# Kernel tuning notes

Hardware: AMD Instinct MI355X
Metric: run time of the kernel (lower is better)

The kernel has to match this reference:

```python
import jax, jax.numpy as jnp
import numpy as np

N_CELLS = 500_000
B = 512
D_X = 128
D_Z = 32
D_IN = D_X + D_Z  # 160
H = 256
D_OUT = 16


def _linear_params(key, fan_in, fan_out):
    k1, k2 = jax.random.split(key)
    bound = 1.0 / np.sqrt(fan_in)
    W = jax.random.uniform(k1, (fan_in, fan_out), jnp.float32, -bound, bound)
    b = jax.random.uniform(k2, (fan_out,), jnp.float32, -bound, bound)
    return W, b


def setup_inputs() -> dict:
    key = jax.random.key(0)
    ks = jax.random.split(key, 8)
    X = jax.random.uniform(ks[0], (N_CELLS, D_X), jnp.float32)  # nonneg counts-like
    Z = jax.random.normal(ks[1], (B, D_Z), jnp.float32)
    cell_to_batch = jax.random.randint(ks[2], (N_CELLS,), 0, B, jnp.int64)
    sample_idx_batch = jnp.arange(B, dtype=jnp.int64)
    W1, b1 = _linear_params(ks[3], D_IN, H)
    W2, b2 = _linear_params(ks[4], H, H)
    W3, b3 = _linear_params(ks[5], H, D_OUT)
    return {"X": X, "Z": Z, "W1": W1, "b1": b1, "W2": W2, "b2": b2,
            "W3": W3, "b3": b3, "cell_to_batch": cell_to_batch,
            "sample_idx_batch": sample_idx_batch}


def reference(X, Z, W1, b1, W2, b2, W3, b3, cell_to_batch, sample_idx_batch):
    # gather per-sample covariates to per-cell rows
    Zc = Z[cell_to_batch]                              # [N, D_Z]
    seg = sample_idx_batch[cell_to_batch]              # [N] remapped sample ids
    # preprocessor: log-normalize X, concat covariates
    Xp = jnp.concatenate([jnp.log1p(X), Zc], axis=-1)  # [N, D_IN]
    # cell predictor MLP (Linear-ReLU x2 + Linear)
    h = jax.nn.relu(Xp @ W1 + b1)
    h = jax.nn.relu(h @ W2 + b2)
    X_cell = h @ W3 + b3                               # [N, D_OUT]
    # aggregator: segment mean over cells of each sample
    nseg = sample_idx_batch.shape[0]
    sums = jax.ops.segment_sum(X_cell, seg, num_segments=nseg)
    counts = jax.ops.segment_sum(jnp.ones((X_cell.shape[0], 1), X_cell.dtype), seg, num_segments=nseg)
    Y_sample = sums / jnp.maximum(counts, 1.0)
    # postprocessor: identity
    return Y_sample
```

## Files before the change

### kernel.cpp

```cpp
#include <hip/hip_runtime.h>
#include <hip/hip_bf16.h>

typedef __attribute__((ext_vector_type(8))) short short8;
typedef __attribute__((ext_vector_type(4))) short short4v;
typedef __attribute__((ext_vector_type(4))) float floatx4;

#define N_CELLS  500000
#define B_SAMP   512
#define D_X      128
#define D_Z      32
#define D_IN     160
#define H_DIM    256
#define D_OUT    16

#define M_TILE   64
#define NBLK     7813
#define LDH      264

#define NREP     64

#define OFF_W1P   0
#define OFF_W2P   81920
#define OFF_W3P   212992
#define OFF_ACC   221184
#define OFF_CNT   2318336

#define ZERO_BLKS 2176
#define W1_BLKS   160
#define W2_BLKS   256
#define W3_BLKS   16

__device__ __forceinline__ short bfb(float x) {
    union { __hip_bfloat16 h; short s; } u;
    u.h = __float2bfloat16(x);
    return u.s;
}

__global__ __launch_bounds__(256)
void prep(const float* __restrict__ W1, const float* __restrict__ W2,
          const float* __restrict__ W3,
          __hip_bfloat16* __restrict__ w1p, __hip_bfloat16* __restrict__ w2p,
          __hip_bfloat16* __restrict__ w3p, float* __restrict__ accs) {
    int bid = blockIdx.x;
    if (bid < ZERO_BLKS) {
        accs[bid * 256 + threadIdx.x] = 0.0f;
        return;
    }
    const float* W; __hip_bfloat16* dst; int N, kS, idx, scaleK;
    if (bid < ZERO_BLKS + W1_BLKS) {
        idx = (bid - ZERO_BLKS) * 256 + threadIdx.x;
        W = W1; dst = w1p; N = H_DIM; kS = 5; scaleK = 128;
    } else if (bid < ZERO_BLKS + W1_BLKS + W2_BLKS) {
        idx = (bid - ZERO_BLKS - W1_BLKS) * 256 + threadIdx.x;
        W = W2; dst = w2p; N = H_DIM; kS = 8; scaleK = 0;
    } else {
        idx = (bid - ZERO_BLKS - W1_BLKS - W2_BLKS) * 256 + threadIdx.x;
        W = W3; dst = w3p; N = D_OUT; kS = 8; scaleK = 0;
    }
    int j = idx & 7;
    int L = (idx >> 3) & 63;
    int s = (idx >> 9) % kS;
    int t = idx / (kS << 9);
    int k = s * 32 + ((L >> 4) << 3) + j;
    int n = t * 16 + (L & 15);
    float v = W[(size_t)k * N + n];
    if (k < scaleK) v *= 0.6931471805599453f;
    dst[idx] = __float2bfloat16(v);
}

__global__ __launch_bounds__(512, 4)
void fused_mlp(const float* __restrict__ X, const float* __restrict__ Z,
               const int* __restrict__ c2b, const int* __restrict__ sidx,
               const float* __restrict__ b1, const float* __restrict__ b2,
               const float* __restrict__ b3,
               const __hip_bfloat16* __restrict__ w1p,
               const __hip_bfloat16* __restrict__ w2p,
               const __hip_bfloat16* __restrict__ w3p,
               float* __restrict__ accs, float* __restrict__ cnts) {
    __shared__ __hip_bfloat16 sA[M_TILE][LDH];
    __shared__ __hip_bfloat16 sB[M_TILE][LDH];

    const int tid = threadIdx.x;
    const int w   = tid >> 6;
    const int L   = tid & 63;
    const int q   = L >> 4;
    const int ln  = L & 15;
    const int wm  = w >> 2;
    const int wn  = w & 3;
    const int base = blockIdx.x * M_TILE;

#pragma unroll
    for (int i = 0; i < 4; ++i) {
        int idx = tid + i * 512;
        int row = idx >> 5;
        int c4  = idx & 31;
        int gr = base + row; if (gr >= N_CELLS) gr = N_CELLS - 1;
        float4 v = *(const float4*)(X + (size_t)gr * D_X + c4 * 4);
        short4v pk;
        pk.x = bfb(__log2f(1.0f + v.x));
        pk.y = bfb(__log2f(1.0f + v.y));
        pk.z = bfb(__log2f(1.0f + v.z));
        pk.w = bfb(__log2f(1.0f + v.w));
        *(short4v*)&sA[row][c4 * 4] = pk;
    }
    {
        int row = tid >> 3;
        int c0  = (tid & 7) * 4;
        int gr = base + row; if (gr >= N_CELLS) gr = N_CELLS - 1;
        int b  = c2b[gr];
        float4 v = *(const float4*)(Z + (size_t)b * D_Z + c0);
        short4v pk;
        pk.x = bfb(v.x); pk.y = bfb(v.y); pk.z = bfb(v.z); pk.w = bfb(v.w);
        *(short4v*)&sA[row][D_X + c0] = pk;
    }
    __syncthreads();

    floatx4 acc[2][4];

#pragma unroll
    for (int nt = 0; nt < 4; ++nt) {
        float4 bv = *(const float4*)(b1 + wn * 64 + nt * 16 + q * 4);
        acc[0][nt] = (floatx4){bv.x, bv.y, bv.z, bv.w};
        acc[1][nt] = acc[0][nt];
    }
#pragma unroll
    for (int s = 0; s < 5; ++s) {
        short8 x0 = *(const short8*)&sA[wm * 32 + ln][s * 32 + q * 8];
        short8 x1 = *(const short8*)&sA[wm * 32 + 16 + ln][s * 32 + q * 8];
#pragma unroll
        for (int nt = 0; nt < 4; ++nt) {
            int t = wn * 4 + nt;
            short8 wf = *(const short8*)(w1p + (size_t)(((t * 5 + s) << 6) + L) * 8);
            acc[0][nt] = __builtin_amdgcn_mfma_f32_16x16x32_bf16(wf, x0, acc[0][nt], 0, 0, 0);
            acc[1][nt] = __builtin_amdgcn_mfma_f32_16x16x32_bf16(wf, x1, acc[1][nt], 0, 0, 0);
        }
    }
#pragma unroll
    for (int mt = 0; mt < 2; ++mt)
#pragma unroll
        for (int nt = 0; nt < 4; ++nt) {
            short4v pk;
            pk.x = bfb(fmaxf(acc[mt][nt][0], 0.0f));
            pk.y = bfb(fmaxf(acc[mt][nt][1], 0.0f));
            pk.z = bfb(fmaxf(acc[mt][nt][2], 0.0f));
            pk.w = bfb(fmaxf(acc[mt][nt][3], 0.0f));
            *(short4v*)&sB[wm * 32 + mt * 16 + ln][wn * 64 + nt * 16 + q * 4] = pk;
        }
    __syncthreads();

#pragma unroll
    for (int nt = 0; nt < 4; ++nt) {
        float4 bv = *(const float4*)(b2 + wn * 64 + nt * 16 + q * 4);
        acc[0][nt] = (floatx4){bv.x, bv.y, bv.z, bv.w};
        acc[1][nt] = acc[0][nt];
    }
#pragma unroll
    for (int s = 0; s < 8; ++s) {
        short8 x0 = *(const short8*)&sB[wm * 32 + ln][s * 32 + q * 8];
        short8 x1 = *(const short8*)&sB[wm * 32 + 16 + ln][s * 32 + q * 8];
#pragma unroll
        for (int nt = 0; nt < 4; ++nt) {
            int t = wn * 4 + nt;
            short8 wf = *(const short8*)(w2p + (size_t)(((t * 8 + s) << 6) + L) * 8);
            acc[0][nt] = __builtin_amdgcn_mfma_f32_16x16x32_bf16(wf, x0, acc[0][nt], 0, 0, 0);
            acc[1][nt] = __builtin_amdgcn_mfma_f32_16x16x32_bf16(wf, x1, acc[1][nt], 0, 0, 0);
        }
    }
#pragma unroll
    for (int mt = 0; mt < 2; ++mt)
#pragma unroll
        for (int nt = 0; nt < 4; ++nt) {
            short4v pk;
            pk.x = bfb(fmaxf(acc[mt][nt][0], 0.0f));
            pk.y = bfb(fmaxf(acc[mt][nt][1], 0.0f));
            pk.z = bfb(fmaxf(acc[mt][nt][2], 0.0f));
            pk.w = bfb(fmaxf(acc[mt][nt][3], 0.0f));
            *(short4v*)&sA[wm * 32 + mt * 16 + ln][wn * 64 + nt * 16 + q * 4] = pk;
        }
    __syncthreads();

    if (w < 4) {
        float4 bv = *(const float4*)(b3 + q * 4);
        floatx4 a3 = (floatx4){bv.x, bv.y, bv.z, bv.w};
#pragma unroll
        for (int s = 0; s < 8; ++s) {
            short8 h  = *(const short8*)&sA[w * 16 + ln][s * 32 + q * 8];
            short8 wf = *(const short8*)(w3p + (size_t)((s << 6) + L) * 8);
            a3 = __builtin_amdgcn_mfma_f32_16x16x32_bf16(wf, h, a3, 0, 0, 0);
        }
        int cell = base + w * 16 + ln;
        if (cell < N_CELLS) {
            int b = c2b[cell];
            int so = sidx[b];
            int rep = blockIdx.x & (NREP - 1);
            float* dst = accs + (size_t)rep * (B_SAMP * D_OUT) + (size_t)so * D_OUT + q * 4;
            atomicAdd(dst + 0, a3[0]);
            atomicAdd(dst + 1, a3[1]);
            atomicAdd(dst + 2, a3[2]);
            atomicAdd(dst + 3, a3[3]);
            if (q == 0) atomicAdd(cnts + (size_t)rep * B_SAMP + so, 1.0f);
        }
    }
}

__global__ __launch_bounds__(256)
void finalize(const float* __restrict__ accs, const float* __restrict__ cnts,
              float* __restrict__ out) {
    int o = blockIdx.x * blockDim.x + threadIdx.x;
    int s = o >> 4;
    float sum = 0.f, cnt = 0.f;
#pragma unroll 8
    for (int r = 0; r < NREP; ++r) {
        sum += accs[(size_t)r * (B_SAMP * D_OUT) + o];
        cnt += cnts[(size_t)r * B_SAMP + s];
    }
    out[o] = sum / fmaxf(cnt, 1.0f);
}

extern "C" void kernel_launch(void* const* d_in, const int* in_sizes, int n_in,
                              void* d_out, int out_size, void* d_ws, size_t ws_size,
                              hipStream_t stream) {
    const float* X   = (const float*)d_in[0];
    const float* Z   = (const float*)d_in[1];
    const float* W1  = (const float*)d_in[2];
    const float* b1  = (const float*)d_in[3];
    const float* W2  = (const float*)d_in[4];
    const float* b2  = (const float*)d_in[5];
    const float* W3  = (const float*)d_in[6];
    const float* b3  = (const float*)d_in[7];
    const int*   c2b = (const int*)d_in[8];
    const int*   sidx= (const int*)d_in[9];

    char* ws = (char*)d_ws;
    __hip_bfloat16* w1p = (__hip_bfloat16*)(ws + OFF_W1P);
    __hip_bfloat16* w2p = (__hip_bfloat16*)(ws + OFF_W2P);
    __hip_bfloat16* w3p = (__hip_bfloat16*)(ws + OFF_W3P);
    float* accs = (float*)(ws + OFF_ACC);
    float* cnts = (float*)(ws + OFF_CNT);
    float* out  = (float*)d_out;

    prep<<<ZERO_BLKS + W1_BLKS + W2_BLKS + W3_BLKS, 256, 0, stream>>>(
        W1, W2, W3, w1p, w2p, w3p, accs);

    fused_mlp<<<NBLK, 512, 0, stream>>>(X, Z, c2b, sidx, b1, b2, b3,
                                        w1p, w2p, w3p, accs, cnts);
    finalize<<<32, 256, 0, stream>>>(accs, cnts, out);
}
```

Before: 492.7 us.

## Precompute Z·W1 per sample, persistent blocks with X prefetch, split layer-3 K across waves

```diff
diff --git a/kernel.cpp b/kernel.cpp
--- a/kernel.cpp
+++ b/kernel.cpp
@@ -9,26 +9,32 @@
 #define B_SAMP   512
 #define D_X      128
 #define D_Z      32
-#define D_IN     160
 #define H_DIM    256
 #define D_OUT    16
 
 #define M_TILE   64
-#define NBLK     7813
+#define NT       7813
+#define NPBLK    512
+#define LDA      136
 #define LDH      264
+#define SP_LD    20
 
 #define NREP     64
 
 #define OFF_W1P   0
-#define OFF_W2P   81920
-#define OFF_W3P   212992
-#define OFF_ACC   221184
-#define OFF_CNT   2318336
+#define OFF_W2P   65536
+#define OFF_W3P   196608
+#define OFF_ZW    204800
+#define OFF_ACC   729088
+#define OFF_CNT   2826240
+#define OFF_C2S   2957312
 
 #define ZERO_BLKS 2176
-#define W1_BLKS   160
+#define W1_BLKS   128
 #define W2_BLKS   256
 #define W3_BLKS   16
+#define ZW_BLKS   512
+#define C2S_BLKS  1954
 
 __device__ __forceinline__ short bfb(float x) {
     union { __hip_bfloat16 h; short s; } u;
@@ -37,48 +43,69 @@
 }
 
 __global__ __launch_bounds__(256)
-void prep(const float* __restrict__ W1, const float* __restrict__ W2,
-          const float* __restrict__ W3,
+void prep(const float* __restrict__ W1, const float* __restrict__ b1,
+          const float* __restrict__ W2, const float* __restrict__ W3,
+          const float* __restrict__ Z,
+          const int* __restrict__ c2b, const int* __restrict__ sidx,
           __hip_bfloat16* __restrict__ w1p, __hip_bfloat16* __restrict__ w2p,
-          __hip_bfloat16* __restrict__ w3p, float* __restrict__ accs) {
+          __hip_bfloat16* __restrict__ w3p, float* __restrict__ zw1,
+          float* __restrict__ accs, int* __restrict__ c2s) {
     int bid = blockIdx.x;
-    if (bid < ZERO_BLKS) {
-        accs[bid * 256 + threadIdx.x] = 0.0f;
+    int tid = threadIdx.x;
+    if (bid < ZERO_BLKS) { accs[bid * 256 + tid] = 0.0f; return; }
+    bid -= ZERO_BLKS;
+    if (bid < W1_BLKS + W2_BLKS + W3_BLKS) {
+        const float* W; __hip_bfloat16* dst; int N, kS, idx; float scale;
+        if (bid < W1_BLKS) {
+            idx = bid * 256 + tid; W = W1; dst = w1p; N = H_DIM; kS = 4;
+            scale = 0.6931471805599453f;
+        } else if (bid < W1_BLKS + W2_BLKS) {
+            idx = (bid - W1_BLKS) * 256 + tid; W = W2; dst = w2p; N = H_DIM; kS = 8;
+            scale = 1.0f;
+        } else {
+            idx = (bid - W1_BLKS - W2_BLKS) * 256 + tid; W = W3; dst = w3p; N = D_OUT; kS = 8;
+            scale = 1.0f;
+        }
+        int j = idx & 7;
+        int L = (idx >> 3) & 63;
+        int s = (idx >> 9) % kS;
+        int t = idx / (kS << 9);
+        int k = s * 32 + ((L >> 4) << 3) + j;
+        int n = t * 16 + (L & 15);
+        dst[idx] = __float2bfloat16(W[(size_t)k * N + n] * scale);
         return;
     }
-    const float* W; __hip_bfloat16* dst; int N, kS, idx, scaleK;
-    if (bid < ZERO_BLKS + W1_BLKS) {
-        idx = (bid - ZERO_BLKS) * 256 + threadIdx.x;
-        W = W1; dst = w1p; N = H_DIM; kS = 5; scaleK = 128;
-    } else if (bid < ZERO_BLKS + W1_BLKS + W2_BLKS) {
-        idx = (bid - ZERO_BLKS - W1_BLKS) * 256 + threadIdx.x;
-        W = W2; dst = w2p; N = H_DIM; kS = 8; scaleK = 0;
-    } else {
-        idx = (bid - ZERO_BLKS - W1_BLKS - W2_BLKS) * 256 + threadIdx.x;
-        W = W3; dst = w3p; N = D_OUT; kS = 8; scaleK = 0;
-    }
-    int j = idx & 7;
-    int L = (idx >> 3) & 63;
-    int s = (idx >> 9) % kS;
-    int t = idx / (kS << 9);
-    int k = s * 32 + ((L >> 4) << 3) + j;
-    int n = t * 16 + (L & 15);
-    float v = W[(size_t)k * N + n];
-    if (k < scaleK) v *= 0.6931471805599453f;
-    dst[idx] = __float2bfloat16(v);
+    bid -= W1_BLKS + W2_BLKS + W3_BLKS;
+    if (bid < ZW_BLKS) {
+        int s = bid;
+        float a = b1[tid];
+        const float* zr = Z + (size_t)s * D_Z;
+        const float* wr = W1 + (size_t)D_X * H_DIM + tid;
+#pragma unroll 8
+        for (int k = 0; k < D_Z; ++k) a += zr[k] * wr[(size_t)k * H_DIM];
+        zw1[(size_t)s * H_DIM + tid] = a;
+        return;
+    }
+    bid -= ZW_BLKS;
+    int i = bid * 256 + tid;
+    if (i < N_CELLS) c2s[i] = sidx[c2b[i]];
 }
 
 __global__ __launch_bounds__(512, 4)
-void fused_mlp(const float* __restrict__ X, const float* __restrict__ Z,
-               const int* __restrict__ c2b, const int* __restrict__ sidx,
-               const float* __restrict__ b1, const float* __restrict__ b2,
+void fused_mlp(const float* __restrict__ X, const int* __restrict__ c2b,
+               const int* __restrict__ c2s, const float* __restrict__ b2,
                const float* __restrict__ b3,
                const __hip_bfloat16* __restrict__ w1p,
                const __hip_bfloat16* __restrict__ w2p,
                const __hip_bfloat16* __restrict__ w3p,
+               const float* __restrict__ zw1,
                float* __restrict__ accs, float* __restrict__ cnts) {
-    __shared__ __hip_bfloat16 sA[M_TILE][LDH];
-    __shared__ __hip_bfloat16 sB[M_TILE][LDH];
+    __shared__ __align__(16) short sX[M_TILE * LDA];
+    __shared__ short sH[M_TILE][LDH];
+    __shared__ int sCB[M_TILE];
+    __shared__ int sSI[M_TILE];
+    short (*xp)[LDA] = (short (*)[LDA])sX;
+    float (*sP)[M_TILE][SP_LD] = (float (*)[M_TILE][SP_LD])sX;
 
     const int tid = threadIdx.x;
     const int w   = tid >> 6;
@@ -87,119 +114,168 @@
     const int ln  = L & 15;
     const int wm  = w >> 2;
     const int wn  = w & 3;
-    const int base = blockIdx.x * M_TILE;
-
-#pragma unroll
-    for (int i = 0; i < 4; ++i) {
-        int idx = tid + i * 512;
-        int row = idx >> 5;
-        int c4  = idx & 31;
-        int gr = base + row; if (gr >= N_CELLS) gr = N_CELLS - 1;
-        float4 v = *(const float4*)(X + (size_t)gr * D_X + c4 * 4);
-        short4v pk;
-        pk.x = bfb(__log2f(1.0f + v.x));
-        pk.y = bfb(__log2f(1.0f + v.y));
-        pk.z = bfb(__log2f(1.0f + v.z));
-        pk.w = bfb(__log2f(1.0f + v.w));
-        *(short4v*)&sA[row][c4 * 4] = pk;
-    }
+
+    float4 xr[4];
+    int cb = 0, si = 0;
+
+    int t = blockIdx.x;
     {
-        int row = tid >> 3;
-        int c0  = (tid & 7) * 4;
-        int gr = base + row; if (gr >= N_CELLS) gr = N_CELLS - 1;
-        int b  = c2b[gr];
-        float4 v = *(const float4*)(Z + (size_t)b * D_Z + c0);
-        short4v pk;
-        pk.x = bfb(v.x); pk.y = bfb(v.y); pk.z = bfb(v.z); pk.w = bfb(v.w);
-        *(short4v*)&sA[row][D_X + c0] = pk;
-    }
-    __syncthreads();
-
-    floatx4 acc[2][4];
-
-#pragma unroll
-    for (int nt = 0; nt < 4; ++nt) {
-        float4 bv = *(const float4*)(b1 + wn * 64 + nt * 16 + q * 4);
-        acc[0][nt] = (floatx4){bv.x, bv.y, bv.z, bv.w};
-        acc[1][nt] = acc[0][nt];
-    }
-#pragma unroll
-    for (int s = 0; s < 5; ++s) {
-        short8 x0 = *(const short8*)&sA[wm * 32 + ln][s * 32 + q * 8];
-        short8 x1 = *(const short8*)&sA[wm * 32 + 16 + ln][s * 32 + q * 8];
+        int base = t * M_TILE;
+#pragma unroll
+        for (int i = 0; i < 4; ++i) {
+            int idx = tid + i * 512;
+            int gr = base + (idx >> 5); if (gr >= N_CELLS) gr = N_CELLS - 1;
+            xr[i] = *(const float4*)(X + (size_t)gr * D_X + (idx & 31) * 4);
+        }
+        if ((tid & 7) == 0) {
+            int gr = base + (tid >> 3); if (gr >= N_CELLS) gr = N_CELLS - 1;
+            cb = c2b[gr];
+            si = c2s[gr];
+        }
+    }
+
+    for (; t < NT; t += NPBLK) {
+        const int base = t * M_TILE;
+
+#pragma unroll
+        for (int i = 0; i < 4; ++i) {
+            int idx = tid + i * 512;
+            int row = idx >> 5, c4 = idx & 31;
+            short4v pk;
+            pk.x = bfb(__log2f(1.0f + xr[i].x));
+            pk.y = bfb(__log2f(1.0f + xr[i].y));
+            pk.z = bfb(__log2f(1.0f + xr[i].z));
+            pk.w = bfb(__log2f(1.0f + xr[i].w));
+            *(short4v*)&xp[row][c4 * 4] = pk;
+        }
+        if ((tid & 7) == 0) { sCB[tid >> 3] = cb; sSI[tid >> 3] = si; }
+        __syncthreads();
+
+        if (t + NPBLK < NT) {
+            int nb = (t + NPBLK) * M_TILE;
+#pragma unroll
+            for (int i = 0; i < 4; ++i) {
+                int idx = tid + i * 512;
+                int gr = nb + (idx >> 5); if (gr >= N_CELLS) gr = N_CELLS - 1;
+                xr[i] = *(const float4*)(X + (size_t)gr * D_X + (idx & 31) * 4);
+            }
+            if ((tid & 7) == 0) {
+                int gr = nb + (tid >> 3); if (gr >= N_CELLS) gr = N_CELLS - 1;
+                cb = c2b[gr];
+                si = c2s[gr];
+            }
+        }
+
+        int cb0 = sCB[wm * 32 + ln];
+        int cb1 = sCB[wm * 32 + 16 + ln];
+        float4 zwa[4], zwb[4];
 #pragma unroll
         for (int nt = 0; nt < 4; ++nt) {
-            int t = wn * 4 + nt;
-            short8 wf = *(const short8*)(w1p + (size_t)(((t * 5 + s) << 6) + L) * 8);
-            acc[0][nt] = __builtin_amdgcn_mfma_f32_16x16x32_bf16(wf, x0, acc[0][nt], 0, 0, 0);
-            acc[1][nt] = __builtin_amdgcn_mfma_f32_16x16x32_bf16(wf, x1, acc[1][nt], 0, 0, 0);
-        }
-    }
-#pragma unroll
-    for (int mt = 0; mt < 2; ++mt)
+            zwa[nt] = *(const float4*)(zw1 + (size_t)cb0 * H_DIM + wn * 64 + nt * 16 + q * 4);
+            zwb[nt] = *(const float4*)(zw1 + (size_t)cb1 * H_DIM + wn * 64 + nt * 16 + q * 4);
+        }
+        floatx4 acc[2][4];
+#pragma unroll
+        for (int mt = 0; mt < 2; ++mt)
+#pragma unroll
+            for (int nt = 0; nt < 4; ++nt)
+                acc[mt][nt] = (floatx4){0.f, 0.f, 0.f, 0.f};
+#pragma unroll
+        for (int s = 0; s < 4; ++s) {
+            short8 x0 = *(const short8*)&xp[wm * 32 + ln][s * 32 + q * 8];
+            short8 x1 = *(const short8*)&xp[wm * 32 + 16 + ln][s * 32 + q * 8];
+#pragma unroll
+            for (int nt = 0; nt < 4; ++nt) {
+                short8 wf = *(const short8*)(w1p + (size_t)(((((wn * 4 + nt) * 4) + s) << 6) + L) * 8);
+                acc[0][nt] = __builtin_amdgcn_mfma_f32_16x16x32_bf16(wf, x0, acc[0][nt], 0, 0, 0);
+                acc[1][nt] = __builtin_amdgcn_mfma_f32_16x16x32_bf16(wf, x1, acc[1][nt], 0, 0, 0);
+            }
+        }
 #pragma unroll
         for (int nt = 0; nt < 4; ++nt) {
-            short4v pk;
-            pk.x = bfb(fmaxf(acc[mt][nt][0], 0.0f));
-            pk.y = bfb(fmaxf(acc[mt][nt][1], 0.0f));
-            pk.z = bfb(fmaxf(acc[mt][nt][2], 0.0f));
-            pk.w = bfb(fmaxf(acc[mt][nt][3], 0.0f));
-            *(short4v*)&sB[wm * 32 + mt * 16 + ln][wn * 64 + nt * 16 + q * 4] = pk;
-        }
-    __syncthreads();
-
-#pragma unroll
-    for (int nt = 0; nt < 4; ++nt) {
-        float4 bv = *(const float4*)(b2 + wn * 64 + nt * 16 + q * 4);
-        acc[0][nt] = (floatx4){bv.x, bv.y, bv.z, bv.w};
-        acc[1][nt] = acc[0][nt];
-    }
-#pragma unroll
-    for (int s = 0; s < 8; ++s) {
-        short8 x0 = *(const short8*)&sB[wm * 32 + ln][s * 32 + q * 8];
-        short8 x1 = *(const short8*)&sB[wm * 32 + 16 + ln][s * 32 + q * 8];
+            short4v p0, p1;
+            p0.x = bfb(fmaxf(acc[0][nt][0] + zwa[nt].x, 0.f));
+            p0.y = bfb(fmaxf(acc[0][nt][1] + zwa[nt].y, 0.f));
+            p0.z = bfb(fmaxf(acc[0][nt][2] + zwa[nt].z, 0.f));
+            p0.w = bfb(fmaxf(acc[0][nt][3] + zwa[nt].w, 0.f));
+            p1.x = bfb(fmaxf(acc[1][nt][0] + zwb[nt].x, 0.f));
+            p1.y = bfb(fmaxf(acc[1][nt][1] + zwb[nt].y, 0.f));
+            p1.z = bfb(fmaxf(acc[1][nt][2] + zwb[nt].z, 0.f));
+            p1.w = bfb(fmaxf(acc[1][nt][3] + zwb[nt].w, 0.f));
+            *(short4v*)&sH[wm * 32 + ln][wn * 64 + nt * 16 + q * 4] = p0;
+            *(short4v*)&sH[wm * 32 + 16 + ln][wn * 64 + nt * 16 + q * 4] = p1;
+        }
+        __syncthreads();
+
 #pragma unroll
         for (int nt = 0; nt < 4; ++nt) {
-            int t = wn * 4 + nt;
-            short8 wf = *(const short8*)(w2p + (size_t)(((t * 8 + s) << 6) + L) * 8);
-            acc[0][nt] = __builtin_amdgcn_mfma_f32_16x16x32_bf16(wf, x0, acc[0][nt], 0, 0, 0);
-            acc[1][nt] = __builtin_amdgcn_mfma_f32_16x16x32_bf16(wf, x1, acc[1][nt], 0, 0, 0);
-        }
-    }
-#pragma unroll
-    for (int mt = 0; mt < 2; ++mt)
+            float4 bv = *(const float4*)(b2 + wn * 64 + nt * 16 + q * 4);
+            acc[0][nt] = (floatx4){bv.x, bv.y, bv.z, bv.w};
+            acc[1][nt] = acc[0][nt];
+        }
+#pragma unroll
+        for (int s = 0; s < 8; ++s) {
+            short8 x0 = *(const short8*)&sH[wm * 32 + ln][s * 32 + q * 8];
+            short8 x1 = *(const short8*)&sH[wm * 32 + 16 + ln][s * 32 + q * 8];
+#pragma unroll
+            for (int nt = 0; nt < 4; ++nt) {
+                short8 wf = *(const short8*)(w2p + (size_t)(((((wn * 4 + nt) * 8) + s) << 6) + L) * 8);
+                acc[0][nt] = __builtin_amdgcn_mfma_f32_16x16x32_bf16(wf, x0, acc[0][nt], 0, 0, 0);
+                acc[1][nt] = __builtin_amdgcn_mfma_f32_16x16x32_bf16(wf, x1, acc[1][nt], 0, 0, 0);
+            }
+        }
+        __syncthreads();
 #pragma unroll
         for (int nt = 0; nt < 4; ++nt) {
-            short4v pk;
-            pk.x = bfb(fmaxf(acc[mt][nt][0], 0.0f));
-            pk.y = bfb(fmaxf(acc[mt][nt][1], 0.0f));
-            pk.z = bfb(fmaxf(acc[mt][nt][2], 0.0f));
-            pk.w = bfb(fmaxf(acc[mt][nt][3], 0.0f));
-            *(short4v*)&sA[wm * 32 + mt * 16 + ln][wn * 64 + nt * 16 + q * 4] = pk;
-        }
-    __syncthreads();
-
-    if (w < 4) {
-        float4 bv = *(const float4*)(b3 + q * 4);
-        floatx4 a3 = (floatx4){bv.x, bv.y, bv.z, bv.w};
-#pragma unroll
-        for (int s = 0; s < 8; ++s) {
-            short8 h  = *(const short8*)&sA[w * 16 + ln][s * 32 + q * 8];
-            short8 wf = *(const short8*)(w3p + (size_t)((s << 6) + L) * 8);
-            a3 = __builtin_amdgcn_mfma_f32_16x16x32_bf16(wf, h, a3, 0, 0, 0);
-        }
-        int cell = base + w * 16 + ln;
-        if (cell < N_CELLS) {
-            int b = c2b[cell];
-            int so = sidx[b];
-            int rep = blockIdx.x & (NREP - 1);
-            float* dst = accs + (size_t)rep * (B_SAMP * D_OUT) + (size_t)so * D_OUT + q * 4;
-            atomicAdd(dst + 0, a3[0]);
-            atomicAdd(dst + 1, a3[1]);
-            atomicAdd(dst + 2, a3[2]);
-            atomicAdd(dst + 3, a3[3]);
-            if (q == 0) atomicAdd(cnts + (size_t)rep * B_SAMP + so, 1.0f);
-        }
+            short4v p0, p1;
+            p0.x = bfb(fmaxf(acc[0][nt][0], 0.f));
+            p0.y = bfb(fmaxf(acc[0][nt][1], 0.f));
+            p0.z = bfb(fmaxf(acc[0][nt][2], 0.f));
+            p0.w = bfb(fmaxf(acc[0][nt][3], 0.f));
+            p1.x = bfb(fmaxf(acc[1][nt][0], 0.f));
+            p1.y = bfb(fmaxf(acc[1][nt][1], 0.f));
+            p1.z = bfb(fmaxf(acc[1][nt][2], 0.f));
+            p1.w = bfb(fmaxf(acc[1][nt][3], 0.f));
+            *(short4v*)&sH[wm * 32 + ln][wn * 64 + nt * 16 + q * 4] = p0;
+            *(short4v*)&sH[wm * 32 + 16 + ln][wn * 64 + nt * 16 + q * 4] = p1;
+        }
+        __syncthreads();
+
+        {
+            int g  = w & 3;
+            int kh = w >> 2;
+            floatx4 a3 = (floatx4){0.f, 0.f, 0.f, 0.f};
+#pragma unroll
+            for (int ss = 0; ss < 4; ++ss) {
+                int s = kh * 4 + ss;
+                short8 hv = *(const short8*)&sH[g * 16 + ln][s * 32 + q * 8];
+                short8 wf = *(const short8*)(w3p + (size_t)(((s) << 6) + L) * 8);
+                a3 = __builtin_amdgcn_mfma_f32_16x16x32_bf16(wf, hv, a3, 0, 0, 0);
+            }
+#pragma unroll
+            for (int r = 0; r < 4; ++r)
+                sP[kh][g * 16 + ln][q * 4 + r] = a3[r];
+        }
+        __syncthreads();
+
+        {
+            int rep = ((t >> 9) + t) & (NREP - 1);
+            float* accR = accs + (size_t)rep * (B_SAMP * D_OUT);
+            float* cntR = cnts + (size_t)rep * B_SAMP;
+#pragma unroll
+            for (int i = 0; i < 2; ++i) {
+                int idx = tid + i * 512;
+                int m = idx >> 4, n = idx & 15;
+                int cell = base + m;
+                if (cell < N_CELLS) {
+                    float v = sP[0][m][n] + sP[1][m][n] + b3[n];
+                    int so = sSI[m];
+                    atomicAdd(&accR[(size_t)so * D_OUT + n], v);
+                    if (n == 0) atomicAdd(&cntR[so], 1.0f);
+                }
+            }
+        }
+        __syncthreads();
     }
 }
 
@@ -235,14 +311,16 @@
     __hip_bfloat16* w1p = (__hip_bfloat16*)(ws + OFF_W1P);
     __hip_bfloat16* w2p = (__hip_bfloat16*)(ws + OFF_W2P);
     __hip_bfloat16* w3p = (__hip_bfloat16*)(ws + OFF_W3P);
+    float* zw1  = (float*)(ws + OFF_ZW);
     float* accs = (float*)(ws + OFF_ACC);
     float* cnts = (float*)(ws + OFF_CNT);
+    int*   c2s  = (int*)(ws + OFF_C2S);
     float* out  = (float*)d_out;
 
-    prep<<<ZERO_BLKS + W1_BLKS + W2_BLKS + W3_BLKS, 256, 0, stream>>>(
-        W1, W2, W3, w1p, w2p, w3p, accs);
-
-    fused_mlp<<<NBLK, 512, 0, stream>>>(X, Z, c2b, sidx, b1, b2, b3,
-                                        w1p, w2p, w3p, accs, cnts);
+    prep<<<ZERO_BLKS + W1_BLKS + W2_BLKS + W3_BLKS + ZW_BLKS + C2S_BLKS, 256, 0, stream>>>(
+        W1, b1, W2, W3, Z, c2b, sidx, w1p, w2p, w3p, zw1, accs, c2s);
+
+    fused_mlp<<<NPBLK, 512, 0, stream>>>(X, c2b, c2s, b2, b3,
+                                         w1p, w2p, w3p, zw1, accs, cnts);
     finalize<<<32, 256, 0, stream>>>(accs, cnts, out);
 }
```

Measured after the change: 1.046 ms. +112.4%, slower.
